# Performance work log

Measured on AMD Instinct MI355X. Metric: run time of the kernel, lower is better.

## Reference

```python
import jax, jax.numpy as jnp
import numpy as np

D = 384        # residual_depth
QK = 48        # D // qk_dim_div(=8)
E = 768        # D * expand_factor(=2)
NB = 8         # num_blocks
VOCAB = 100
LN_EPS = 1e-5


def _ln(x, g, b):
    m = x.mean(-1, keepdims=True)
    v = x.var(-1, keepdims=True)  # biased, matches torch LayerNorm
    return (x - m) / jnp.sqrt(v + LN_EPS) * g + b


def setup_inputs() -> dict:
    key = jax.random.key(0)
    ks = jax.random.split(key, 5)
    B, S = 4, 2048
    q = jax.random.randint(ks[0], (B, S), 0, 100, dtype=jnp.int32)
    freqs = jnp.exp(jnp.arange(0, D, 2, dtype=jnp.float32) * (-np.log(10000.0) / D))
    # fused expand: rows = qk + qk + expand + expand = 1632
    exp_w = (0.5 / np.sqrt(D) / 2.0) * jax.random.normal(ks[1], (NB, 2 * QK + 2 * E, D), dtype=jnp.float32)
    proj_w = (1.0 / np.sqrt(D) / 2.0 / NB) * jax.random.normal(ks[2], (NB, D, E), dtype=jnp.float32)
    blk_g = jnp.ones((NB, D), jnp.float32)
    blk_b = jnp.zeros((NB, D), jnp.float32)
    ln_g = jnp.ones((D,), jnp.float32)
    ln_b = jnp.zeros((D,), jnp.float32)
    out_w = 0.02 * jax.random.normal(ks[3], (VOCAB, D), dtype=jnp.float32)
    return dict(q=q, freqs=freqs, exp_w=exp_w, proj_w=proj_w,
                blk_g=blk_g, blk_b=blk_b, ln_g=ln_g, ln_b=ln_b, out_w=out_w)


def reference(q, freqs, exp_w, proj_w, blk_g, blk_b, ln_g, ln_b, out_w):
    S = q.shape[1]
    # sinusoidal encoding of integer tokens -> [B,S,D]
    qe = q.astype(jnp.float32)[..., None] * freqs
    x = jnp.concatenate([jnp.sin(qe), jnp.cos(qe)], axis=-1)
    x = _ln(x, ln_g, ln_b)
    # causal mask; position_bias_base is zeros in the source
    bias = jnp.where(jnp.tril(jnp.ones((S, S), bool)), 0.0, -jnp.inf).astype(jnp.float32)
    inv_sqrt_qk = 1.0 / np.sqrt(QK)

    def block(x, p):
        ew, pw, g, b = p
        xn = _ln(x, g, b)
        h = xn @ ew.T                                   # [B,S,1632]
        qh, kh, lin, pg = jnp.split(h, [QK, 2 * QK, 2 * QK + E], axis=-1)
        geglu = lin * jax.nn.gelu(pg, approximate=False)  # [B,S,E]
        loc, val = geglu[..., :E - D], geglu[..., E - D:]  # [B,S,D],[B,S,D]
        sc = jnp.einsum('bqd,bkd->bqk', qh, kh) * inv_sqrt_qk + bias
        attn = jax.nn.softmax(sc, axis=-1) @ val          # [B,S,D]
        out = jnp.concatenate([loc, attn], axis=-1) @ pw.T
        return x + out, None

    x, _ = jax.lax.scan(block, x, (exp_w, proj_w, blk_g, blk_b))
    x = _ln(x, ln_g, ln_b)
    return x @ out_w.T
```

## Files before the change

kernel.cpp:

```cpp
#include <hip/hip_runtime.h>
#include <hip/hip_bf16.h>

#define TOK 8192
#define DM 384
#define QKD 48
#define EM 768
#define NBLK 8
#define NVOCAB 100
#define SEQ 2048
#define HN 1664
#define HNV 1632
#define CH 8
#define NUNITS 2304

using short4v = __attribute__((ext_vector_type(4))) short;
using short8 = __attribute__((ext_vector_type(8))) short;
using f32x4  = __attribute__((ext_vector_type(4))) float;

static __device__ __forceinline__ float bf2f(short s) {
    union { unsigned u; float f; } c; c.u = ((unsigned)(unsigned short)s) << 16; return c.f;
}
static __device__ __forceinline__ short f2bf(float f) {
    union { float f; unsigned u; } c; c.f = f;
    unsigned r = (c.u + 0x7FFFu + ((c.u >> 16) & 1u)) >> 16;
    return (short)r;
}
static __device__ __forceinline__ void gload_lds16(const short* g, short* l) {
    __builtin_amdgcn_global_load_lds((const __attribute__((address_space(1))) void*)g,
                                     (__attribute__((address_space(3))) void*)l, 16, 0, 0);
}

__global__ __launch_bounds__(256) void k_setup(const float* __restrict__ expw,
        const float* __restrict__ projw, const float* __restrict__ outw,
        short* __restrict__ ewb, short* __restrict__ pwb, short* __restrict__ owb,
        const int* __restrict__ q, const float* __restrict__ freqs,
        const float* __restrict__ lng, const float* __restrict__ lnb,
        const float* __restrict__ bg0, const float* __restrict__ bb0,
        float* __restrict__ x, short* __restrict__ xn) {
    const int n1 = NBLK * HN * DM;
    for (int i = blockIdx.x * 256 + threadIdx.x; i < n1; i += gridDim.x * 256) {
        int L = i / (HN * DM); int rem = i % (HN * DM);
        int r = rem / DM; int c = rem % DM;
        float v = (r < HNV) ? expw[((size_t)L * HNV + r) * DM + c] : 0.f;
        ewb[i] = f2bf(v);
    }
    const int n2 = NBLK * DM * EM;
    for (int i = blockIdx.x * 256 + threadIdx.x; i < n2; i += gridDim.x * 256)
        pwb[i] = f2bf(projw[i]);
    const int n3 = 128 * DM;
    for (int i = blockIdx.x * 256 + threadIdx.x; i < n3; i += gridDim.x * 256) {
        int r = i / DM, c = i % DM;
        owb[i] = f2bf(r < NVOCAB ? outw[r * DM + c] : 0.f);
    }
    int wid = blockIdx.x * 4 + (threadIdx.x >> 6);
    int lane = threadIdx.x & 63;
    float qv = (float)q[wid];
    float v[6]; float s = 0.f, s2 = 0.f;
    #pragma unroll
    for (int i = 0; i < 6; ++i) {
        int d = lane + 64 * i;
        float val;
        if (d < 192) val = sinf(qv * freqs[d]);
        else         val = cosf(qv * freqs[d - 192]);
        v[i] = val; s += val; s2 += val * val;
    }
    #pragma unroll
    for (int m = 1; m < 64; m <<= 1) { s += __shfl_xor(s, m); s2 += __shfl_xor(s2, m); }
    float mean = s * (1.f / DM);
    float var = s2 * (1.f / DM) - mean * mean;
    float rstd = rsqrtf(var + 1e-5f);
    float* xr = x + (size_t)wid * DM;
    float s3 = 0.f, s4 = 0.f;
    #pragma unroll
    for (int i = 0; i < 6; ++i) {
        int d = lane + 64 * i;
        v[i] = (v[i] - mean) * rstd * lng[d] + lnb[d];
        xr[d] = v[i];
        s3 += v[i]; s4 += v[i] * v[i];
    }
    #pragma unroll
    for (int m = 1; m < 64; m <<= 1) { s3 += __shfl_xor(s3, m); s4 += __shfl_xor(s4, m); }
    float mean2 = s3 * (1.f / DM);
    float var2 = s4 * (1.f / DM) - mean2 * mean2;
    float rstd2 = rsqrtf(var2 + 1e-5f);
    short* xo = xn + (size_t)wid * DM;
    #pragma unroll
    for (int i = 0; i < 6; ++i) {
        int d = lane + 64 * i;
        xo[d] = f2bf((v[i] - mean2) * rstd2 * bg0[d] + bb0[d]);
    }
}

__global__ __launch_bounds__(256) void k_gemmh(const short* __restrict__ A,
        const short* __restrict__ Bw, short* __restrict__ cat,
        short* __restrict__ vT, short* __restrict__ qhb, short* __restrict__ khb) {
    __shared__ __align__(16) short As[128 * 64];
    __shared__ __align__(16) short Bs[128 * 64];
    int m0 = blockIdx.x * 128;
    int y = blockIdx.y;
    int t = threadIdx.x;
    int wid = t >> 6, lane = t & 63;
    int wm = (wid >> 1) * 64, wn = (wid & 1) * 64;
    int lr = lane & 15, lg = lane >> 4;
    int srow = wid * 32 + (lane >> 3);
    int sck = (lane & 7) ^ (lane >> 3);
    auto bmap = [&](int row) {
        if (y < 12) {
            int sh = row >> 4;
            return 96 + (sh & 1) * 768 + y * 64 + (sh >> 1) * 16 + (row & 15);
        }
        return (row < 96) ? row : 1632 + (row - 96);
    };
    const short* srcA[4]; const short* srcB[4]; short* dstA[4]; short* dstB[4];
    #pragma unroll
    for (int i = 0; i < 4; ++i) {
        int row = srow + i * 8;
        srcA[i] = A + (size_t)(m0 + row) * DM + sck * 8;
        srcB[i] = Bw + (size_t)bmap(row) * DM + sck * 8;
        dstA[i] = As + wid * 2048 + i * 512;
        dstB[i] = Bs + wid * 2048 + i * 512;
    }
    const f32x4 vz = {0.f, 0.f, 0.f, 0.f};
    f32x4 acc[4][4];
    #pragma unroll
    for (int i = 0; i < 4; ++i)
        #pragma unroll
        for (int j = 0; j < 4; ++j) acc[i][j] = vz;
    for (int k0 = 0; k0 < DM; k0 += 64) {
        if (k0) __syncthreads();
        #pragma unroll
        for (int i = 0; i < 4; ++i) {
            gload_lds16(srcA[i] + k0, dstA[i]);
            gload_lds16(srcB[i] + k0, dstB[i]);
        }
        __syncthreads();
        #pragma unroll
        for (int ks = 0; ks < 2; ++ks) {
            short8 af[4], bfr[4];
            #pragma unroll
            for (int i = 0; i < 4; ++i) {
                int ra = wm + i * 16 + lr;
                int rb = wn + i * 16 + lr;
                af[i]  = *(const short8*)(As + ra * 64 + (((lg + ks * 4) ^ (ra & 7)) * 8));
                bfr[i] = *(const short8*)(Bs + rb * 64 + (((lg + ks * 4) ^ (rb & 7)) * 8));
            }
            #pragma unroll
            for (int i = 0; i < 4; ++i)
                #pragma unroll
                for (int j = 0; j < 4; ++j)
                    acc[i][j] = __builtin_amdgcn_mfma_f32_16x16x32_bf16(af[i], bfr[j], acc[i][j], 0, 0, 0);
        }
    }
    if (y < 12) {
        #pragma unroll
        for (int i = 0; i < 4; ++i) {
            int tok0 = m0 + wm + i * 16 + lg * 4;
            #pragma unroll
            for (int k = 0; k < 2; ++k) {
                int e = y * 64 + (wn >> 1) + k * 16 + lr;
                short vb[4];
                #pragma unroll
                for (int r = 0; r < 4; ++r) {
                    float l = acc[i][2 * k][r], pg = acc[i][2 * k + 1][r];
                    float gel = pg * 0.5f * (1.f + erff(pg * 0.70710678118654752f));
                    vb[r] = f2bf(l * gel);
                }
                if (y < 6) {
                    #pragma unroll
                    for (int r = 0; r < 4; ++r)
                        cat[(size_t)(tok0 + r) * EM + e] = vb[r];
                } else {
                    short4v pk = {vb[0], vb[1], vb[2], vb[3]};
                    *(short4v*)(vT + (size_t)(e - DM) * TOK + tok0) = pk;
                }
            }
        }
    } else {
        #pragma unroll
        for (int i = 0; i < 4; ++i)
            #pragma unroll
            for (int j = 0; j < 4; ++j) {
                int col = wn + j * 16 + lr;
                #pragma unroll
                for (int r = 0; r < 4; ++r) {
                    int tok = m0 + wm + i * 16 + lg * 4 + r;
                    short v = f2bf(acc[i][j][r]);
                    if (col < 64) qhb[(size_t)tok * 64 + col] = (col < QKD) ? v : (short)0;
                    if (col >= QKD && col < QKD + 64)
                        khb[(size_t)tok * 64 + col - QKD] = (col < 96) ? v : (short)0;
                }
            }
    }
}

template<int MODE>
__global__ __launch_bounds__(256) void k_gemm(const short* __restrict__ A,
        const short* __restrict__ Bw, int K, int lda, int ldb,
        void* __restrict__ Cp, int ldc) {
    __shared__ __align__(16) short As[128 * 32];
    __shared__ __align__(16) short Bs[128 * 32];
    int m0 = blockIdx.x * 128, n0 = blockIdx.y * 128;
    int t = threadIdx.x;
    int wid = t >> 6, lane = t & 63;
    int wm = (wid >> 1) * 64, wn = (wid & 1) * 64;
    int lr = lane & 15, lg = lane >> 4;
    int seg0 = wid * 2, seg1 = wid * 2 + 1;
    int row0 = seg0 * 16 + (lane >> 2), row1 = seg1 * 16 + (lane >> 2);
    int cu0 = (lane & 3) ^ ((row0 + (row0 >> 2)) & 3);
    int cu1 = (lane & 3) ^ ((row1 + (row1 >> 2)) & 3);
    const short* srcA0 = A + (size_t)(m0 + row0) * lda + cu0 * 8;
    const short* srcA1 = A + (size_t)(m0 + row1) * lda + cu1 * 8;
    const short* srcB0 = Bw + (size_t)(n0 + row0) * ldb + cu0 * 8;
    const short* srcB1 = Bw + (size_t)(n0 + row1) * ldb + cu1 * 8;
    short* dA0 = As + seg0 * 512; short* dA1 = As + seg1 * 512;
    short* dB0 = Bs + seg0 * 512; short* dB1 = Bs + seg1 * 512;
    const f32x4 vz = {0.f, 0.f, 0.f, 0.f};
    f32x4 acc[4][4];
    #pragma unroll
    for (int i = 0; i < 4; ++i)
        #pragma unroll
        for (int j = 0; j < 4; ++j) acc[i][j] = vz;
    for (int k0 = 0; k0 < K; k0 += 32) {
        if (k0) __syncthreads();
        gload_lds16(srcA0 + k0, dA0);
        gload_lds16(srcA1 + k0, dA1);
        gload_lds16(srcB0 + k0, dB0);
        gload_lds16(srcB1 + k0, dB1);
        __syncthreads();
        short8 af[4], bfr[4];
        #pragma unroll
        for (int i = 0; i < 4; ++i) {
            int ra = wm + i * 16 + lr;
            int rb = wn + i * 16 + lr;
            af[i]  = *(const short8*)(As + ra * 32 + ((lg ^ ((ra + (ra >> 2)) & 3)) * 8));
            bfr[i] = *(const short8*)(Bs + rb * 32 + ((lg ^ ((rb + (rb >> 2)) & 3)) * 8));
        }
        #pragma unroll
        for (int i = 0; i < 4; ++i)
            #pragma unroll
            for (int j = 0; j < 4; ++j)
                acc[i][j] = __builtin_amdgcn_mfma_f32_16x16x32_bf16(af[i], bfr[j], acc[i][j], 0, 0, 0);
    }
    int rb = m0 + wm + (lane >> 4) * 4;
    int cb = n0 + wn + lr;
    #pragma unroll
    for (int i = 0; i < 4; ++i)
        #pragma unroll
        for (int j = 0; j < 4; ++j)
            #pragma unroll
            for (int r = 0; r < 4; ++r) {
                int row = rb + i * 16 + r;
                int col = cb + j * 16;
                float v = acc[i][j][r];
                if (MODE == 0) ((short*)Cp)[(size_t)row * ldc + col] = f2bf(v);
                else if (MODE == 1) ((float*)Cp)[(size_t)row * ldc + col] += v;
                else if (col < NVOCAB) ((float*)Cp)[(size_t)row * NVOCAB + col] = v;
            }
}

__global__ __launch_bounds__(256) void k_gemmproj(const short* __restrict__ A,
        const short* __restrict__ Bw, float* __restrict__ x,
        short* __restrict__ xn, const float* __restrict__ g,
        const float* __restrict__ b) {
    __shared__ __align__(16) short As[32 * 32];
    __shared__ __align__(16) short Bs[384 * 32];
    __shared__ float redS[4][32];
    __shared__ float redQ[4][32];
    int m0 = blockIdx.x * 32;
    int t = threadIdx.x;
    int wid = t >> 6, lane = t & 63;
    int lr = lane & 15, lg = lane >> 4;
    const short* src[7]; short* dst[7]; bool valid[7];
    int rin = lane >> 2, cch = lane & 3;
    #pragma unroll
    for (int qd = 0; qd < 7; ++qd) {
        int seg = wid * 7 + qd;
        valid[qd] = (seg < 26);
        int segc = valid[qd] ? seg : 25;
        if (segc < 2) {
            int row = segc * 16 + rin;
            int cu = cch ^ ((row + (row >> 2)) & 3);
            src[qd] = A + (size_t)(m0 + row) * EM + cu * 8;
            dst[qd] = As + segc * 512;
        } else {
            int row = (segc - 2) * 16 + rin;
            int cu = cch ^ ((row + (row >> 2)) & 3);
            src[qd] = Bw + (size_t)row * EM + cu * 8;
            dst[qd] = Bs + (segc - 2) * 512;
        }
    }
    const f32x4 vz = {0.f, 0.f, 0.f, 0.f};
    f32x4 acc[2][6];
    #pragma unroll
    for (int i = 0; i < 2; ++i)
        #pragma unroll
        for (int j = 0; j < 6; ++j) acc[i][j] = vz;
    for (int k0 = 0; k0 < EM; k0 += 32) {
        if (k0) __syncthreads();
        #pragma unroll
        for (int qd = 0; qd < 7; ++qd)
            if (valid[qd]) gload_lds16(src[qd] + k0, dst[qd]);
        __syncthreads();
        short8 af[2], bfr[6];
        #pragma unroll
        for (int i = 0; i < 2; ++i) {
            int ra = i * 16 + lr;
            af[i] = *(const short8*)(As + ra * 32 + ((lg ^ ((ra + (ra >> 2)) & 3)) * 8));
        }
        #pragma unroll
        for (int j = 0; j < 6; ++j) {
            int rb = wid * 96 + j * 16 + lr;
            bfr[j] = *(const short8*)(Bs + rb * 32 + ((lg ^ ((rb + (rb >> 2)) & 3)) * 8));
        }
        #pragma unroll
        for (int i = 0; i < 2; ++i)
            #pragma unroll
            for (int j = 0; j < 6; ++j)
                acc[i][j] = __builtin_amdgcn_mfma_f32_16x16x32_bf16(af[i], bfr[j], acc[i][j], 0, 0, 0);
    }
    #pragma unroll
    for (int i = 0; i < 2; ++i) {
        float rs[4], rq[4];
        #pragma unroll
        for (int r = 0; r < 4; ++r) {
            int row = m0 + i * 16 + lg * 4 + r;
            float s = 0.f, q2 = 0.f;
            #pragma unroll
            for (int j = 0; j < 6; ++j) {
                int col = wid * 96 + j * 16 + lr;
                float yv = x[(size_t)row * DM + col] + acc[i][j][r];
                acc[i][j][r] = yv;
                s += yv; q2 += yv * yv;
            }
            #pragma unroll
            for (int m = 1; m < 16; m <<= 1) { s += __shfl_xor(s, m); q2 += __shfl_xor(q2, m); }
            rs[r] = s; rq[r] = q2;
        }
        if (lr == 0) {
            #pragma unroll
            for (int r = 0; r < 4; ++r) {
                redS[wid][i * 16 + lg * 4 + r] = rs[r];
                redQ[wid][i * 16 + lg * 4 + r] = rq[r];
            }
        }
    }
    __syncthreads();
    #pragma unroll
    for (int i = 0; i < 2; ++i)
        #pragma unroll
        for (int r = 0; r < 4; ++r) {
            int lrow = i * 16 + lg * 4 + r;
            float s = redS[0][lrow] + redS[1][lrow] + redS[2][lrow] + redS[3][lrow];
            float q2 = redQ[0][lrow] + redQ[1][lrow] + redQ[2][lrow] + redQ[3][lrow];
            float mean = s * (1.f / DM);
            float var = q2 * (1.f / DM) - mean * mean;
            float rstd = rsqrtf(var + 1e-5f);
            int row = m0 + lrow;
            #pragma unroll
            for (int j = 0; j < 6; ++j) {
                int col = wid * 96 + j * 16 + lr;
                float yv = acc[i][j][r];
                x[(size_t)row * DM + col] = yv;
                xn[(size_t)row * DM + col] = f2bf((yv - mean) * rstd * g[col] + b[col]);
            }
        }
}

__global__ __launch_bounds__(256) void k_flash(const short* __restrict__ qhb,
        const short* __restrict__ khb, const short* __restrict__ vT,
        short* __restrict__ Po, float* __restrict__ Pml) {
    int idx = blockIdx.x;
    int xcd = idx & 7;
    int b = xcd >> 1;
    int unit = ((idx >> 3) << 1) | (xcd & 1);
    int gq = unit & 31, c = unit >> 5;
    if (c > (gq >> 2)) return;
    __shared__ __align__(16) short Vlds[384 * 40];
    __shared__ __align__(16) short Klds[32 * 64];
    __shared__ __align__(16) short Plds[4 * 16 * 40];
    int t = threadIdx.x;
    int wid = t >> 6, lane = t & 63;
    int lr = lane & 15, lg = lane >> 4;
    int qt = gq * 4 + wid;
    int g = qt >> 4;
    int tb = b * SEQ;
    int q0 = qt * 16;
    int nkbm = 2 * gq + 2;
    int kb0 = c * CH;
    int kb1 = min(kb0 + CH, nkbm);
    short* P = Plds + wid * (16 * 40);
    const float scale = 0.14433756729740643f;
    const float CFIX = 8.f;
    const f32x4 vzero = {0.f, 0.f, 0.f, 0.f};

    short8 qf[2];
    #pragma unroll
    for (int ks = 0; ks < 2; ++ks)
        qf[ks] = *(const short8*)(qhb + (size_t)(tb + q0 + lr) * 64 + ks * 32 + lg * 8);

    f32x4 o[24];
    #pragma unroll
    for (int j = 0; j < 24; ++j) o[j] = vzero;
    float li[4];
    #pragma unroll
    for (int r = 0; r < 4; ++r) li[r] = 0.f;

    int vrow = t >> 2, vc = (t & 3) * 8;
    const short* vsrc0 = vT + (size_t)vrow * TOK + tb + vc;
    int krow = t >> 3, kc8 = (t & 7) * 8;
    const short* ksrc0 = khb + (size_t)(tb + krow) * 64 + kc8;

    short8 rv[6], rk;
    #pragma unroll
    for (int i = 0; i < 6; ++i)
        rv[i] = *(const short8*)(vsrc0 + (size_t)(i * 64) * TOK + kb0 * 32);
    rk = *(const short8*)(ksrc0 + (size_t)kb0 * 2048);

    for (int kb = kb0; kb < kb1; ++kb) {
        int kbase = kb * 32;
        __syncthreads();
        #pragma unroll
        for (int i = 0; i < 6; ++i)
            *(short8*)(Vlds + (vrow + i * 64) * 40 + vc) = rv[i];
        *(short8*)(Klds + krow * 64 + kc8) = rk;
        if (kb + 1 < kb1) {
            #pragma unroll
            for (int i = 0; i < 6; ++i)
                rv[i] = *(const short8*)(vsrc0 + (size_t)(i * 64) * TOK + kbase + 32);
            rk = *(const short8*)(ksrc0 + (size_t)(kb + 1) * 2048);
        }
        __syncthreads();
        short8 kf0a = *(const short8*)(Klds + lr * 64 + lg * 8);
        short8 kf0b = *(const short8*)(Klds + lr * 64 + 32 + lg * 8);
        short8 kf1a = *(const short8*)(Klds + (16 + lr) * 64 + lg * 8);
        short8 kf1b = *(const short8*)(Klds + (16 + lr) * 64 + 32 + lg * 8);

        f32x4 s0 = vzero, s1 = vzero;
        s0 = __builtin_amdgcn_mfma_f32_16x16x32_bf16(qf[0], kf0a, s0, 0, 0, 0);
        s0 = __builtin_amdgcn_mfma_f32_16x16x32_bf16(qf[1], kf0b, s0, 0, 0, 0);
        s1 = __builtin_amdgcn_mfma_f32_16x16x32_bf16(qf[0], kf1a, s1, 0, 0, 0);
        s1 = __builtin_amdgcn_mfma_f32_16x16x32_bf16(qf[1], kf1b, s1, 0, 0, 0);

        bool needmask = (kbase + 31 > q0);
        #pragma unroll
        for (int r = 0; r < 4; ++r) {
            float v0 = s0[r] * scale, v1 = s1[r] * scale;
            if (needmask) {
                int qg = q0 + lg * 4 + r;
                if (kbase + lr > qg) v0 = -1e30f;
                if (kbase + 16 + lr > qg) v1 = -1e30f;
            }
            float p0 = __expf(v0 - CFIX);
            float p1 = __expf(v1 - CFIX);
            li[r] += p0 + p1;
            s0[r] = p0; s1[r] = p1;
        }
        #pragma unroll
        for (int r = 0; r < 4; ++r) {
            P[(lg * 4 + r) * 40 + lr] = f2bf(s0[r]);
            P[(lg * 4 + r) * 40 + 16 + lr] = f2bf(s1[r]);
        }
        short8 pf = *(const short8*)(P + lr * 40 + lg * 8);
        #pragma unroll
        for (int j = 0; j < 24; ++j) {
            short8 vf = *(const short8*)(Vlds + (j * 16 + lr) * 40 + lg * 8);
            o[j] = __builtin_amdgcn_mfma_f32_16x16x32_bf16(pf, vf, o[j], 0, 0, 0);
        }
    }
    #pragma unroll
    for (int r = 0; r < 4; ++r) {
        float sum = li[r];
        #pragma unroll
        for (int d2 = 1; d2 < 16; d2 <<= 1) sum += __shfl_xor(sum, d2);
        li[r] = sum;
    }
    int uid = 8 * g * (g + 1) + (qt & 15) * (g + 1) + c;
    int sidx = (uid << 2) | b;
    size_t ob = (size_t)sidx * (16 * 384);
    #pragma unroll
    for (int j = 0; j < 24; ++j)
        #pragma unroll
        for (int r = 0; r < 4; ++r)
            Po[ob + (size_t)(lg * 4 + r) * 384 + j * 16 + lr] = f2bf(o[j][r]);
    if (lr == 0) {
        #pragma unroll
        for (int r = 0; r < 4; ++r)
            Pml[sidx * 32 + 16 + lg * 4 + r] = li[r];
    }
}

__global__ __launch_bounds__(256) void k_comb(const short* __restrict__ Po,
        const float* __restrict__ Pml, short* __restrict__ cat) {
    int bid = blockIdx.x;
    int b = bid & 3, qt = bid >> 2;
    int g = qt >> 4;
    int nch = g + 1;
    int ubase = 8 * g * (g + 1) + (qt & 15) * (g + 1);
    int tid = threadIdx.x;
    int row = tid >> 4;
    int c0 = (tid & 15) * 24;
    float L = 0.f;
    float acc[24];
    #pragma unroll
    for (int e = 0; e < 24; ++e) acc[e] = 0.f;
    #pragma unroll
    for (int c = 0; c < 8; ++c) {
        if (c < nch) {
            int uu = ((ubase + c) << 2) | b;
            L += Pml[uu * 32 + 16 + row];
            const short8* pp = (const short8*)(Po + ((size_t)uu * 16 + row) * 384 + c0);
            #pragma unroll
            for (int v = 0; v < 3; ++v) {
                short8 tv = pp[v];
                #pragma unroll
                for (int k = 0; k < 8; ++k) acc[v * 8 + k] += bf2f(tv[k]);
            }
        }
    }
    float invL = 1.f / L;
    size_t tok = (size_t)b * SEQ + qt * 16 + row;
    short* dst = cat + tok * EM + DM + c0;
    #pragma unroll
    for (int v = 0; v < 3; ++v) {
        short8 o8;
        #pragma unroll
        for (int k = 0; k < 8; ++k) o8[k] = f2bf(acc[v * 8 + k] * invL);
        *(short8*)(dst + v * 8) = o8;
    }
}

extern "C" void kernel_launch(void* const* d_in, const int* in_sizes, int n_in,
                              void* d_out, int out_size, void* d_ws, size_t ws_size,
                              hipStream_t stream) {
    const int*   q     = (const int*)d_in[0];
    const float* freqs = (const float*)d_in[1];
    const float* expw  = (const float*)d_in[2];
    const float* projw = (const float*)d_in[3];
    const float* blkg  = (const float*)d_in[4];
    const float* blkb  = (const float*)d_in[5];
    const float* lng   = (const float*)d_in[6];
    const float* lnb   = (const float*)d_in[7];
    const float* outw  = (const float*)d_in[8];
    float* out = (float*)d_out;

    char* p = (char*)d_ws;
    auto alloc = [&](size_t bytes) {
        char* r = p; p += (bytes + 255) & ~(size_t)255; return r;
    };
    float* x   = (float*)alloc((size_t)TOK * DM * 4);
    short* xn  = (short*)alloc((size_t)TOK * DM * 2);
    short* h   = (short*)alloc((size_t)TOK * HN * 2);
    short* cat = (short*)alloc((size_t)TOK * EM * 2);
    short* vT  = (short*)alloc((size_t)DM * TOK * 2);
    short* qhb = (short*)alloc((size_t)TOK * 64 * 2);
    short* khb = (short*)alloc((size_t)TOK * 64 * 2);
    short* ewb = (short*)alloc((size_t)NBLK * HN * DM * 2);
    short* pwb = (short*)alloc((size_t)NBLK * DM * EM * 2);
    short* owb = (short*)alloc((size_t)128 * DM * 2);
    (void)h;
    short* Po  = xn;
    float* Pml = (float*)(Po + (size_t)NUNITS * 16 * 384);

    k_setup<<<2048, 256, 0, stream>>>(expw, projw, outw, ewb, pwb, owb,
                                      q, freqs, lng, lnb, blkg, blkb, x, xn);

    for (int L = 0; L < NBLK; ++L) {
        k_gemmh<<<dim3(64, 13), 256, 0, stream>>>(xn, ewb + (size_t)L * HN * DM,
                                                  cat, vT, qhb, khb);
        k_flash<<<1024, 256, 0, stream>>>(qhb, khb, vT, Po, Pml);
        k_comb<<<512, 256, 0, stream>>>(Po, Pml, cat);
        const float* gn = (L < NBLK - 1) ? blkg + (L + 1) * DM : lng;
        const float* bn = (L < NBLK - 1) ? blkb + (L + 1) * DM : lnb;
        k_gemmproj<<<256, 256, 0, stream>>>(cat, pwb + (size_t)L * DM * EM, x, xn, gn, bn);
    }
    k_gemm<2><<<dim3(64, 1), 256, 0, stream>>>(xn, owb, DM, DM, DM, out, NVOCAB);
}
```

Before: 743.1 us.

## Fuse flash-attention split combine into projection GEMM prologue

Removes the separate k_comb kernel. The projection GEMM now loads its full 32x768 A tile into shared memory: the local half is copied from cat, and the attention half is built by summing the split-KV partials (Po/Pml) and normalizing in-kernel. This saves one launch per layer and a bf16 round trip of the attention output through global memory. In exchange it uses a large shared-memory A buffer, which may lower occupancy, adds a serial prologue before the K loop, and needs separate workspace for Po because xn is now written in the same kernel.

Measured after the change: 685.3 us, median of 2. -7.8%, faster.

```diff
diff --git a/kernel.cpp b/kernel.cpp
--- a/kernel.cpp
+++ b/kernel.cpp
@@ -258,11 +258,12 @@
             }
 }
 
-__global__ __launch_bounds__(256) void k_gemmproj(const short* __restrict__ A,
+__global__ __launch_bounds__(256) void k_gemmproj(const short* __restrict__ cat,
+        const short* __restrict__ Po, const float* __restrict__ Pml,
         const short* __restrict__ Bw, float* __restrict__ x,
         short* __restrict__ xn, const float* __restrict__ g,
         const float* __restrict__ b) {
-    __shared__ __align__(16) short As[32 * 32];
+    __shared__ __align__(16) short Afull[32 * 776];
     __shared__ __align__(16) short Bs[384 * 32];
     __shared__ float redS[4][32];
     __shared__ float redQ[4][32];
@@ -270,24 +271,57 @@
     int t = threadIdx.x;
     int wid = t >> 6, lane = t & 63;
     int lr = lane & 15, lg = lane >> 4;
-    const short* src[7]; short* dst[7]; bool valid[7];
+    int arow = t >> 3, ac0 = (t & 7) * 48;
+    {
+        const short8* src = (const short8*)(cat + (size_t)(m0 + arow) * EM + ac0);
+        short* dst = Afull + arow * 776 + ac0;
+        #pragma unroll
+        for (int i = 0; i < 6; ++i) *(short8*)(dst + i * 8) = src[i];
+    }
+    {
+        int qt = (((m0 >> 4) & 127)) + (arow >> 4);
+        int bA = m0 >> 11;
+        int gg = qt >> 4;
+        int nch = gg + 1;
+        int rowin = arow & 15;
+        int ubase = 8 * gg * (gg + 1) + (qt & 15) * (gg + 1);
+        float accv[48];
+        #pragma unroll
+        for (int e = 0; e < 48; ++e) accv[e] = 0.f;
+        float L = 0.f;
+        #pragma unroll
+        for (int c = 0; c < 8; ++c) {
+            if (c < nch) {
+                int uu = ((ubase + c) << 2) | bA;
+                L += Pml[uu * 32 + 16 + rowin];
+                const short8* pp = (const short8*)(Po + ((size_t)uu * 16 + rowin) * 384 + ac0);
+                #pragma unroll
+                for (int v = 0; v < 6; ++v) {
+                    short8 tv = pp[v];
+                    #pragma unroll
+                    for (int k = 0; k < 8; ++k) accv[v * 8 + k] += bf2f(tv[k]);
+                }
+            }
+        }
+        float invL = 1.f / L;
+        short* dst = Afull + arow * 776 + DM + ac0;
+        #pragma unroll
+        for (int v = 0; v < 6; ++v) {
+            short8 o8;
+            #pragma unroll
+            for (int k = 0; k < 8; ++k) o8[k] = f2bf(accv[v * 8 + k] * invL);
+            *(short8*)(dst + v * 8) = o8;
+        }
+    }
+    const short* srcB[6]; short* dstB[6];
     int rin = lane >> 2, cch = lane & 3;
     #pragma unroll
-    for (int qd = 0; qd < 7; ++qd) {
-        int seg = wid * 7 + qd;
-        valid[qd] = (seg < 26);
-        int segc = valid[qd] ? seg : 25;
-        if (segc < 2) {
-            int row = segc * 16 + rin;
-            int cu = cch ^ ((row + (row >> 2)) & 3);
-            src[qd] = A + (size_t)(m0 + row) * EM + cu * 8;
-            dst[qd] = As + segc * 512;
-        } else {
-            int row = (segc - 2) * 16 + rin;
-            int cu = cch ^ ((row + (row >> 2)) & 3);
-            src[qd] = Bw + (size_t)row * EM + cu * 8;
-            dst[qd] = Bs + (segc - 2) * 512;
-        }
+    for (int qd = 0; qd < 6; ++qd) {
+        int seg = wid * 6 + qd;
+        int row = seg * 16 + rin;
+        int cu = cch ^ ((row + (row >> 2)) & 3);
+        srcB[qd] = Bw + (size_t)row * EM + cu * 8;
+        dstB[qd] = Bs + seg * 512;
     }
     const f32x4 vz = {0.f, 0.f, 0.f, 0.f};
     f32x4 acc[2][6];
@@ -296,17 +330,15 @@
         #pragma unroll
         for (int j = 0; j < 6; ++j) acc[i][j] = vz;
     for (int k0 = 0; k0 < EM; k0 += 32) {
-        if (k0) __syncthreads();
-        #pragma unroll
-        for (int qd = 0; qd < 7; ++qd)
-            if (valid[qd]) gload_lds16(src[qd] + k0, dst[qd]);
+        __syncthreads();
+        #pragma unroll
+        for (int qd = 0; qd < 6; ++qd)
+            gload_lds16(srcB[qd] + k0, dstB[qd]);
         __syncthreads();
         short8 af[2], bfr[6];
         #pragma unroll
-        for (int i = 0; i < 2; ++i) {
-            int ra = i * 16 + lr;
-            af[i] = *(const short8*)(As + ra * 32 + ((lg ^ ((ra + (ra >> 2)) & 3)) * 8));
-        }
+        for (int i = 0; i < 2; ++i)
+            af[i] = *(const short8*)(Afull + (i * 16 + lr) * 776 + k0 + lg * 8);
         #pragma unroll
         for (int j = 0; j < 6; ++j) {
             int rb = wid * 96 + j * 16 + lr;
@@ -489,46 +521,6 @@
     }
 }
 
-__global__ __launch_bounds__(256) void k_comb(const short* __restrict__ Po,
-        const float* __restrict__ Pml, short* __restrict__ cat) {
-    int bid = blockIdx.x;
-    int b = bid & 3, qt = bid >> 2;
-    int g = qt >> 4;
-    int nch = g + 1;
-    int ubase = 8 * g * (g + 1) + (qt & 15) * (g + 1);
-    int tid = threadIdx.x;
-    int row = tid >> 4;
-    int c0 = (tid & 15) * 24;
-    float L = 0.f;
-    float acc[24];
-    #pragma unroll
-    for (int e = 0; e < 24; ++e) acc[e] = 0.f;
-    #pragma unroll
-    for (int c = 0; c < 8; ++c) {
-        if (c < nch) {
-            int uu = ((ubase + c) << 2) | b;
-            L += Pml[uu * 32 + 16 + row];
-            const short8* pp = (const short8*)(Po + ((size_t)uu * 16 + row) * 384 + c0);
-            #pragma unroll
-            for (int v = 0; v < 3; ++v) {
-                short8 tv = pp[v];
-                #pragma unroll
-                for (int k = 0; k < 8; ++k) acc[v * 8 + k] += bf2f(tv[k]);
-            }
-        }
-    }
-    float invL = 1.f / L;
-    size_t tok = (size_t)b * SEQ + qt * 16 + row;
-    short* dst = cat + tok * EM + DM + c0;
-    #pragma unroll
-    for (int v = 0; v < 3; ++v) {
-        short8 o8;
-        #pragma unroll
-        for (int k = 0; k < 8; ++k) o8[k] = f2bf(acc[v * 8 + k] * invL);
-        *(short8*)(dst + v * 8) = o8;
-    }
-}
-
 extern "C" void kernel_launch(void* const* d_in, const int* in_sizes, int n_in,
                               void* d_out, int out_size, void* d_ws, size_t ws_size,
                               hipStream_t stream) {
@@ -549,7 +541,6 @@
     };
     float* x   = (float*)alloc((size_t)TOK * DM * 4);
     short* xn  = (short*)alloc((size_t)TOK * DM * 2);
-    short* h   = (short*)alloc((size_t)TOK * HN * 2);
     short* cat = (short*)alloc((size_t)TOK * EM * 2);
     short* vT  = (short*)alloc((size_t)DM * TOK * 2);
     short* qhb = (short*)alloc((size_t)TOK * 64 * 2);
@@ -557,9 +548,8 @@
     short* ewb = (short*)alloc((size_t)NBLK * HN * DM * 2);
     short* pwb = (short*)alloc((size_t)NBLK * DM * EM * 2);
     short* owb = (short*)alloc((size_t)128 * DM * 2);
-    (void)h;
-    short* Po  = xn;
-    float* Pml = (float*)(Po + (size_t)NUNITS * 16 * 384);
+    short* Po  = (short*)alloc((size_t)NUNITS * 16 * 384 * 2);
+    float* Pml = (float*)alloc((size_t)NUNITS * 32 * 4);
 
     k_setup<<<2048, 256, 0, stream>>>(expw, projw, outw, ewb, pwb, owb,
                                       q, freqs, lng, lnb, blkg, blkb, x, xn);
@@ -568,10 +558,10 @@
         k_gemmh<<<dim3(64, 13), 256, 0, stream>>>(xn, ewb + (size_t)L * HN * DM,
                                                   cat, vT, qhb, khb);
         k_flash<<<1024, 256, 0, stream>>>(qhb, khb, vT, Po, Pml);
-        k_comb<<<512, 256, 0, stream>>>(Po, Pml, cat);
         const float* gn = (L < NBLK - 1) ? blkg + (L + 1) * DM : lng;
         const float* bn = (L < NBLK - 1) ? blkb + (L + 1) * DM : lnb;
-        k_gemmproj<<<256, 256, 0, stream>>>(cat, pwb + (size_t)L * DM * EM, x, xn, gn, bn);
+        k_gemmproj<<<256, 256, 0, stream>>>(cat, Po, Pml, pwb + (size_t)L * DM * EM,
+                                            x, xn, gn, bn);
     }
     k_gemm<2><<<dim3(64, 1), 256, 0, stream>>>(xn, owb, DM, DM, DM, out, NVOCAB);
 }
```
